# Optimization experiments

Measured on AMD Instinct MI355X. Metric: run time of the kernel, lower is better.

The kernel has to match this reference:

```python
import jax, jax.numpy as jnp
import numpy as np
from jax import lax

B, H, W, C = 2, 256, 256, 180
WS, SH, NH = 8, 4, 6
HD = C // NH          # 30
N = WS * WS           # 64
NW = (H // WS) * (W // WS)
HID = 4 * C
SCALE = HD ** -0.5
EPS = 1e-5


def _rel_pos_index(ws):
    coords = np.stack(np.meshgrid(np.arange(ws), np.arange(ws), indexing='ij'))  # [2,ws,ws]
    cf = coords.reshape(2, -1)
    rel = (cf[:, :, None] - cf[:, None, :]).transpose(1, 2, 0)  # [N,N,2]
    rel[:, :, 0] += ws - 1
    rel[:, :, 1] += ws - 1
    rel[:, :, 0] *= 2 * ws - 1
    return rel.sum(-1)  # [N,N]


def _attn_mask(h, w, ws, sh):
    img = np.zeros((h, w))
    sl = (slice(0, -ws), slice(-ws, -sh), slice(-sh, None))
    cnt = 0
    for hs in sl:
        for wsl in sl:
            img[hs, wsl] = cnt
            cnt += 1
    mw = img.reshape(h // ws, ws, w // ws, ws).transpose(0, 2, 1, 3).reshape(-1, ws * ws)  # [nW,N]
    d = mw[:, None, :] - mw[:, :, None]  # [nW,N,N]
    return np.where(d != 0, -100.0, 0.0).astype(np.float32)


REL_IDX = jnp.asarray(_rel_pos_index(WS))          # [N,N] int
MASK = jnp.asarray(_attn_mask(H, W, WS, SH))       # [nW,N,N] float


def _ln(x, g, b):
    m = jnp.mean(x, -1, keepdims=True)
    v = jnp.mean((x - m) ** 2, -1, keepdims=True)
    return (x - m) * lax.rsqrt(v + EPS) * g + b


def _win_part(x):  # (B,H,W,C) -> (B*nW,N,C)
    x = x.reshape(B, H // WS, WS, W // WS, WS, C).transpose(0, 1, 3, 2, 4, 5)
    return x.reshape(-1, N, C)


def _win_rev(w):  # (B*nW,N,C) -> (B,H,W,C)
    x = w.reshape(B, H // WS, W // WS, WS, WS, C).transpose(0, 1, 3, 2, 4, 5)
    return x.reshape(B, H, W, C)


def setup_inputs() -> dict:
    key = jax.random.key(0)
    ks = jax.random.split(key, 8)
    s = 0.02
    return {
        'x': jax.random.normal(ks[0], (B, H * W, C), jnp.float32),
        'norm1_g': jnp.ones((C,), jnp.float32),
        'norm1_b': jnp.zeros((C,), jnp.float32),
        'qkv_w': jax.random.normal(ks[1], (C, 3 * C), jnp.float32) * s,
        'qkv_b': jnp.zeros((3 * C,), jnp.float32),
        'rel_pos_table': jax.random.normal(ks[2], ((2 * WS - 1) ** 2, NH), jnp.float32) * s,
        'proj_w': jax.random.normal(ks[3], (C, C), jnp.float32) * s,
        'proj_b': jnp.zeros((C,), jnp.float32),
        'norm2_g': jnp.ones((C,), jnp.float32),
        'norm2_b': jnp.zeros((C,), jnp.float32),
        'fc1_w': jax.random.normal(ks[4], (C, HID), jnp.float32) * s,
        'fc1_b': jnp.zeros((HID,), jnp.float32),
        'dw_w': jax.random.normal(ks[5], (HID, 1, 3, 3), jnp.float32) * s,
        'dw_b': jnp.zeros((HID,), jnp.float32),
        'fc2_w': jax.random.normal(ks[6], (HID, C), jnp.float32) * s,
        'fc2_b': jnp.zeros((C,), jnp.float32),
    }


def reference(x, norm1_g, norm1_b, qkv_w, qkv_b, rel_pos_table, proj_w, proj_b,
              norm2_g, norm2_b, fc1_w, fc1_b, dw_w, dw_b, fc2_w, fc2_b):
    shortcut = x
    h = _ln(x, norm1_g, norm1_b).reshape(B, H, W, C)
    h = jnp.roll(h, (-SH, -SH), axis=(1, 2))           # cyclic shift
    xw = _win_part(h)                                   # [B*nW, N, C]

    qkv = (xw @ qkv_w + qkv_b).reshape(-1, N, 3, NH, HD).transpose(2, 0, 3, 1, 4)
    q, k, v = qkv[0] * SCALE, qkv[1], qkv[2]            # [B_,NH,N,HD]
    attn = jnp.einsum('bhnd,bhmd->bhnm', q, k)          # [B_,NH,N,N]

    bias = rel_pos_table[REL_IDX.reshape(-1)].reshape(N, N, NH).transpose(2, 0, 1)
    attn = attn + bias[None]
    attn = attn.reshape(B, NW, NH, N, N) + MASK[None, :, None]
    attn = jax.nn.softmax(attn.reshape(-1, NH, N, N), axis=-1)

    out = jnp.einsum('bhnm,bhmd->bhnd', attn, v).transpose(0, 2, 1, 3).reshape(-1, N, C)
    out = out @ proj_w + proj_b
    out = jnp.roll(_win_rev(out), (SH, SH), axis=(1, 2)).reshape(B, H * W, C)
    x = shortcut + out

    # MLP with depthwise-conv interleave
    m = _ln(x, norm2_g, norm2_b)
    m = jax.nn.gelu(m @ fc1_w + fc1_b, approximate=False)   # [B,L,HID]
    mc = m.transpose(0, 2, 1).reshape(B, HID, H, W)
    mc = lax.conv_general_dilated(mc, dw_w, (1, 1), 'SAME',
                                  feature_group_count=HID,
                                  dimension_numbers=('NCHW', 'OIHW', 'NCHW'))
    mc = mc + dw_b[None, :, None, None]
    m = jax.nn.gelu(mc.reshape(B, HID, H * W).transpose(0, 2, 1), approximate=False)
    m = m @ fc2_w + fc2_b
    return x + m
```

## Files before the change

kernel.cpp:

```cpp
#include <hip/hip_runtime.h>
#include <hip/hip_bf16.h>


using short8 = __attribute__((ext_vector_type(8))) short;
using f32x4  = __attribute__((ext_vector_type(4))) float;

constexpr int   ROWS   = 131072;
constexpr float SCALE_ = 0.18257418583505536f;

constexpr size_t OFF_WQ    = 0;
constexpr size_t OFF_WP    = OFF_WQ  + 576*192*2;
constexpr size_t OFF_WF1   = OFF_WP  + 192*192*2;
constexpr size_t OFF_WF2   = OFF_WF1 + 768*192*2;
constexpr size_t OFF_BQ    = OFF_WF2 + 192*736*2;
constexpr size_t OFF_BP    = OFF_BQ  + 576*4;
constexpr size_t OFF_BF1   = OFF_BP  + 192*4;
constexpr size_t OFF_BF2   = OFF_BF1 + 768*4;
constexpr size_t OFF_ZB    = OFF_BF2 + 192*4;
constexpr size_t OFF_BIASF = OFF_ZB  + 192*4;
constexpr size_t OFF_WDWT  = OFF_BIASF + 6*4096*4;
constexpr size_t OFF_BDW   = OFF_WDWT + 9*768*4;
constexpr size_t OFF_R1    = 1048576;
constexpr size_t SZ_R      = (size_t)ROWS * 192 * 2;
constexpr size_t OFF_R2    = OFF_R1 + SZ_R;
constexpr size_t OFF_R3    = OFF_R2 + SZ_R;
constexpr size_t WS_NEEDED = OFF_R3 + SZ_R;
static_assert(OFF_BDW + 768*4 <= OFF_R1, "weights overlap R1");

__device__ __forceinline__ unsigned short f2bf(float f) {
    __hip_bfloat16 h = __float2bfloat16(f);
    return *reinterpret_cast<unsigned short*>(&h);
}
__device__ __forceinline__ float bf2f(unsigned short u) {
    union { unsigned int i; float f; } x; x.i = ((unsigned int)u) << 16; return x.f;
}
__device__ __forceinline__ float gelu_f(float x) {
    return 0.5f * x * (1.0f + erff(x * 0.70710678118654752f));
}

__global__ __launch_bounds__(256) void prep_kernel(
    const float* __restrict__ qkv_w, const float* __restrict__ qkv_b,
    const float* __restrict__ proj_w, const float* __restrict__ proj_b,
    const float* __restrict__ fc1_w, const float* __restrict__ fc1_b,
    const float* __restrict__ fc2_w, const float* __restrict__ fc2_b,
    const float* __restrict__ rpt,
    const float* __restrict__ dw_w, const float* __restrict__ dw_b,
    unsigned short* __restrict__ wq, unsigned short* __restrict__ wp,
    unsigned short* __restrict__ wf1, unsigned short* __restrict__ wf2,
    float* __restrict__ bq, float* __restrict__ bp,
    float* __restrict__ bf1, float* __restrict__ bf2,
    float* __restrict__ zb, float* __restrict__ biasf,
    float* __restrict__ wdwT, float* __restrict__ bdw)
{
    int idx = blockIdx.x * 256 + threadIdx.x;
    constexpr int E1 = 576*192;
    constexpr int E2 = E1 + 192*192;
    constexpr int E3 = E2 + 768*192;
    constexpr int E4 = E3 + 192*736;
    constexpr int E5 = E4 + 576;
    constexpr int E6 = E5 + 192;
    constexpr int E7 = E6 + 768;
    constexpr int E8 = E7 + 192;
    constexpr int E8z = E8 + 192;
    constexpr int E9 = E8z + 6*4096;
    constexpr int E10 = E9 + 9*768;
    constexpr int E11 = E10 + 768;
    if (idx < E1) {
        int n = idx / 192, kx = idx % 192;
        float v = 0.f;
        if (n < 540 && kx < 180) { v = qkv_w[kx*540 + n]; if (n < 180) v *= SCALE_; }
        wq[idx] = f2bf(v);
    } else if (idx < E2) {
        int j = idx - E1; int n = j / 192, kx = j % 192;
        wp[j] = f2bf((n < 180 && kx < 180) ? proj_w[kx*180 + n] : 0.f);
    } else if (idx < E3) {
        int j = idx - E2; int n = j / 192, kx = j % 192;
        wf1[j] = f2bf((n < 720 && kx < 180) ? fc1_w[kx*720 + n] : 0.f);
    } else if (idx < E4) {
        int j = idx - E3; int n = j / 736, kx = j % 736;
        wf2[j] = f2bf((n < 180 && kx < 720) ? fc2_w[kx*180 + n] : 0.f);
    } else if (idx < E5) {
        int n = idx - E4;
        float v = (n < 540) ? qkv_b[n] : 0.f; if (n < 180) v *= SCALE_;
        bq[n] = v;
    } else if (idx < E6) {
        int n = idx - E5; bp[n] = (n < 180) ? proj_b[n] : 0.f;
    } else if (idx < E7) {
        int n = idx - E6; bf1[n] = (n < 720) ? fc1_b[n] : 0.f;
    } else if (idx < E8) {
        int n = idx - E7; bf2[n] = (n < 180) ? fc2_b[n] : 0.f;
    } else if (idx < E8z) {
        zb[idx - E8] = 0.f;
    } else if (idx < E9) {
        int j = idx - E8z;
        int hh = j / 4096, t = j & 4095;
        int n = t >> 6, m = t & 63;
        int rid = ((n>>3) - (m>>3) + 7)*15 + ((n&7) - (m&7) + 7);
        biasf[j] = rpt[rid*6 + hh];
    } else if (idx < E10) {
        int j = idx - E9;
        int tap = j / 768, c = j % 768;
        wdwT[j] = (c < 720) ? dw_w[c*9 + tap] : 0.f;
    } else if (idx < E11) {
        int c = idx - E10;
        bdw[c] = (c < 720) ? dw_b[c] : 0.f;
    }
}

template<int ROLL>
__global__ __launch_bounds__(256) void ln_kernel(const float* __restrict__ x,
    const float* __restrict__ g, const float* __restrict__ bsh,
    unsigned short* __restrict__ out)
{
    int row  = blockIdx.x * 4 + (threadIdx.x >> 6);
    int lane = threadIdx.x & 63;
    size_t src;
    if (ROLL) {
        int b    = row >> 16;
        int widx = (row >> 6) & 1023;
        int n    = row & 63;
        int hr   = ((widx >> 5) << 3) + (n >> 3);
        int wr   = ((widx & 31) << 3) + (n & 7);
        int h2   = (hr + 4) & 255;
        int w2   = (wr + 4) & 255;
        src = ((size_t)b << 16) + (h2 << 8) + w2;
    } else {
        src = (size_t)row;
    }
    const float* xr = x + src * 180;
    float v1 = xr[lane];
    float v2 = xr[lane + 64];
    float v3 = (lane < 52) ? xr[lane + 128] : 0.0f;
    float s1 = v1 + v2 + v3;
    float s2 = v1*v1 + v2*v2 + v3*v3;
    #pragma unroll
    for (int o = 32; o > 0; o >>= 1) { s1 += __shfl_xor(s1, o); s2 += __shfl_xor(s2, o); }
    float mean = s1 * (1.0f/180.0f);
    float var  = s2 * (1.0f/180.0f) - mean*mean;
    float rstd = rsqrtf(var + 1e-5f);
    unsigned short* orow = out + (size_t)row * 192;
    orow[lane]      = f2bf((v1 - mean)*rstd*g[lane]      + bsh[lane]);
    orow[lane + 64] = f2bf((v2 - mean)*rstd*g[lane + 64] + bsh[lane + 64]);
    if (lane < 52) orow[lane + 128] = f2bf((v3 - mean)*rstd*g[lane + 128] + bsh[lane + 128]);
    else           orow[lane + 128] = 0;
}

__global__ __launch_bounds__(256) void zeropad_kernel(unsigned int* q, unsigned int* k, unsigned int* v)
{
    int idx = blockIdx.x * 256 + threadIdx.x;
    int wid = idx / 192, t = idx % 192;
    if (t < 64)       q[wid*1024 + t*16 + 15] = 0;
    else if (t < 128) k[wid*1024 + (t-64)*16 + 15] = 0;
    else              v[wid*1024 + 960 + (t-128)] = 0;
}

template<int MODE>
__global__ __launch_bounds__(256) void gemm64(
    const unsigned short* __restrict__ A, const unsigned short* __restrict__ Bt,
    const float* __restrict__ bias, int K, int lda, int ldb,
    float* __restrict__ out_f, const float* __restrict__ xres,
    unsigned short* __restrict__ oq, unsigned short* __restrict__ ok2,
    unsigned short* __restrict__ ov, unsigned short* __restrict__ obf)
{
    __shared__ __align__(16) unsigned short As[64*40];
    __shared__ __align__(16) unsigned short Bs[64*40];
    const int tid  = threadIdx.x;
    const int bm   = blockIdx.x, bn = blockIdx.y;
    const int lane = tid & 63;
    const int wv   = tid >> 6;
    const int wr   = wv >> 1, wc = wv & 1;
    const int l15  = lane & 15, l4 = lane >> 4;
    const int r    = tid >> 2;
    const int kk   = (tid & 3) << 3;

    f32x4 acc[2][2];
    #pragma unroll
    for (int i = 0; i < 2; i++)
        #pragma unroll
        for (int j = 0; j < 2; j++) acc[i][j] = f32x4{0.f, 0.f, 0.f, 0.f};

    const size_t abase = (size_t)(bm*64 + r) * (size_t)lda + kk;
    const size_t bbase = (size_t)(bn*64 + r) * (size_t)ldb + kk;
    const int lds_wi = r*40 + kk;

    for (int kt = 0; kt < K; kt += 32) {
        *(uint4*)&As[lds_wi] = *(const uint4*)&A[abase + kt];
        *(uint4*)&Bs[lds_wi] = *(const uint4*)&Bt[bbase + kt];
        __syncthreads();
        short8 af[2], bf[2];
        #pragma unroll
        for (int fm = 0; fm < 2; fm++) af[fm] = *(const short8*)&As[(wr*32 + fm*16 + l15)*40 + l4*8];
        #pragma unroll
        for (int fn = 0; fn < 2; fn++) bf[fn] = *(const short8*)&Bs[(wc*32 + fn*16 + l15)*40 + l4*8];
        #pragma unroll
        for (int fm = 0; fm < 2; fm++)
            #pragma unroll
            for (int fn = 0; fn < 2; fn++)
                acc[fm][fn] = __builtin_amdgcn_mfma_f32_16x16x32_bf16(af[fm], bf[fn], acc[fm][fn], 0, 0, 0);
        __syncthreads();
    }

    #pragma unroll
    for (int fm = 0; fm < 2; fm++) {
      #pragma unroll
      for (int fn = 0; fn < 2; fn++) {
        #pragma unroll
        for (int rr = 0; rr < 4; rr++) {
            int row_l = wr*32 + fm*16 + l4*4 + rr;
            int col_l = wc*32 + fn*16 + l15;
            int grow  = bm*64 + row_l;
            int gcol  = bn*64 + col_l;
            float v = acc[fm][fn][rr] + bias[gcol];
            if (MODE == 0) {
                if (gcol < 540) {
                    int which = (gcol >= 360) ? 2 : (gcol >= 180 ? 1 : 0);
                    int cc = gcol - which*180;
                    int hh = cc / 30;
                    int dd = cc - hh*30;
                    size_t wid = (size_t)(grow >> 6)*6 + hh;
                    if (which == 0)      oq [wid*2048 + (grow & 63)*32 + dd] = f2bf(v);
                    else if (which == 1) ok2[wid*2048 + (grow & 63)*32 + dd] = f2bf(v);
                    else                 ov [wid*2048 + dd*64 + (grow & 63)] = f2bf(v);
                }
            } else if (MODE == 1) {
                if (gcol < 180) {
                    int b    = grow >> 16;
                    int widx = (grow >> 6) & 1023;
                    int n    = grow & 63;
                    int hr   = ((widx >> 5) << 3) + (n >> 3);
                    int wr2  = ((widx & 31) << 3) + (n & 7);
                    int h2   = (hr + 4) & 255;
                    int w2   = (wr2 + 4) & 255;
                    size_t orow = ((size_t)b << 16) + (h2 << 8) + w2;
                    out_f[orow*180 + gcol] = xres[orow*180 + gcol] + v;
                }
            } else if (MODE == 2) {
                obf[(size_t)grow*192 + gcol] = f2bf(gelu_f(v));
            } else {
                if (gcol < 180) out_f[(size_t)grow*180 + gcol] += v;
            }
        }
      }
    }
}

__global__ __launch_bounds__(64) void attn_kernel(
    const unsigned short* __restrict__ q, const unsigned short* __restrict__ k,
    const unsigned short* __restrict__ vt, const float* __restrict__ biasf,
    unsigned short* __restrict__ aout)
{
    __shared__ __align__(16) unsigned short P[64*72];
    const int wid  = blockIdx.x;
    const int b_   = wid / 6, hh = wid % 6;
    const int lane = threadIdx.x;
    const int l15  = lane & 15, l4 = lane >> 4;

    const unsigned short* qb = q  + (size_t)wid*2048;
    const unsigned short* kb = k  + (size_t)wid*2048;
    const unsigned short* vb = vt + (size_t)wid*2048;

    short8 qf[4], kf[4];
    #pragma unroll
    for (int t = 0; t < 4; t++) {
        qf[t] = *(const short8*)&qb[(t*16 + l15)*32 + l4*8];
        kf[t] = *(const short8*)&kb[(t*16 + l15)*32 + l4*8];
    }
    f32x4 s[4][4];
    #pragma unroll
    for (int m = 0; m < 4; m++)
        #pragma unroll
        for (int n = 0; n < 4; n++)
            s[m][n] = __builtin_amdgcn_mfma_f32_16x16x32_bf16(qf[m], kf[n], f32x4{0.f,0.f,0.f,0.f}, 0, 0, 0);

    const int wi = b_ & 1023;
    const int wh = wi >> 5, ww = wi & 31;
    const bool edge = (wh == 31) || (ww == 31);
    const float* bh = biasf + hh*4096;
    #pragma unroll
    for (int m = 0; m < 4; m++) {
      #pragma unroll
      for (int rr = 0; rr < 4; rr++) {
        int ni = m*16 + l4*4 + rr;
        int ln_n = 0;
        if (edge) {
            int rh = (wh < 31) ? 0 : (((ni >> 3) < 4) ? 1 : 2);
            int rw = (ww < 31) ? 0 : (((ni & 7) < 4) ? 1 : 2);
            ln_n = rh*3 + rw;
        }
        #pragma unroll
        for (int n = 0; n < 4; n++) {
            int mj = n*16 + l15;
            float add = bh[ni*64 + mj];
            if (edge) {
                int rh = (wh < 31) ? 0 : (((mj >> 3) < 4) ? 1 : 2);
                int rw = (ww < 31) ? 0 : (((mj & 7) < 4) ? 1 : 2);
                if (rh*3 + rw != ln_n) add -= 100.0f;
            }
            s[m][n][rr] += add;
        }
      }
    }
    #pragma unroll
    for (int m = 0; m < 4; m++) {
      #pragma unroll
      for (int rr = 0; rr < 4; rr++) {
        float mx = fmaxf(fmaxf(s[m][0][rr], s[m][1][rr]), fmaxf(s[m][2][rr], s[m][3][rr]));
        #pragma unroll
        for (int o = 8; o > 0; o >>= 1) mx = fmaxf(mx, __shfl_xor(mx, o));
        float sum = 0.f;
        #pragma unroll
        for (int n = 0; n < 4; n++) { float e = __expf(s[m][n][rr] - mx); s[m][n][rr] = e; sum += e; }
        #pragma unroll
        for (int o = 8; o > 0; o >>= 1) sum += __shfl_xor(sum, o);
        float inv = 1.0f / sum;
        int ni = m*16 + l4*4 + rr;
        #pragma unroll
        for (int n = 0; n < 4; n++) P[ni*72 + n*16 + l15] = f2bf(s[m][n][rr] * inv);
      }
    }
    __syncthreads();
    f32x4 po[4][2];
    #pragma unroll
    for (int m = 0; m < 4; m++)
        #pragma unroll
        for (int n = 0; n < 2; n++) po[m][n] = f32x4{0.f,0.f,0.f,0.f};
    #pragma unroll
    for (int ks = 0; ks < 2; ks++) {
        short8 pf[4], vf[2];
        #pragma unroll
        for (int m = 0; m < 4; m++) pf[m] = *(const short8*)&P[(m*16 + l15)*72 + ks*32 + l4*8];
        #pragma unroll
        for (int n = 0; n < 2; n++) vf[n] = *(const short8*)&vb[(n*16 + l15)*64 + ks*32 + l4*8];
        #pragma unroll
        for (int m = 0; m < 4; m++)
            #pragma unroll
            for (int n = 0; n < 2; n++)
                po[m][n] = __builtin_amdgcn_mfma_f32_16x16x32_bf16(pf[m], vf[n], po[m][n], 0, 0, 0);
    }
    #pragma unroll
    for (int m = 0; m < 4; m++)
      #pragma unroll
      for (int n = 0; n < 2; n++)
        #pragma unroll
        for (int rr = 0; rr < 4; rr++) {
            int ni = m*16 + l4*4 + rr;
            int dd = n*16 + l15;
            if (dd < 30)
                aout[((size_t)b_*64 + ni)*192 + hh*30 + dd] = f2bf(po[m][n][rr]);
        }
}

__global__ __launch_bounds__(192) void dwconv_kernel(
    const unsigned short* __restrict__ m1, const float* __restrict__ wT,
    const float* __restrict__ bias, int c0, unsigned short* __restrict__ m2)
{
    const int rowid = blockIdx.x;
    const int b   = rowid >> 8;
    const int hh  = rowid & 255;
    const int t   = threadIdx.x;
    const int cg  = t % 24;
    const int pl  = t / 24;
    const int w0  = blockIdx.y * 64 + pl * 8;
    const int c   = cg * 8;
    const int cgl = c0 + c;

    float acc[8][8];
    float bv[8];
    *(f32x4*)&bv[0] = *(const f32x4*)&bias[cgl];
    *(f32x4*)&bv[4] = *(const f32x4*)&bias[cgl + 4];
    #pragma unroll
    for (int p = 0; p < 8; p++)
        #pragma unroll
        for (int i = 0; i < 8; i++) acc[p][i] = bv[i];

    const short8 zv = {0,0,0,0,0,0,0,0};
    #pragma unroll
    for (int dh = -1; dh <= 1; dh++) {
        int h2 = hh + dh;
        if (h2 < 0 || h2 > 255) continue;
        const unsigned short* rb = m1 + ((size_t)(b*65536 + h2*256))*192 + c;
        float f[10][8];
        #pragma unroll
        for (int j = 0; j < 10; j++) {
            int w2 = w0 - 1 + j;
            short8 v = (w2 < 0 || w2 > 255) ? zv : *(const short8*)&rb[(size_t)w2*192];
            #pragma unroll
            for (int i = 0; i < 8; i++) f[j][i] = bf2f((unsigned short)v[i]);
        }
        #pragma unroll
        for (int dw2 = 0; dw2 < 3; dw2++) {
            const float* wrow = wT + ((dh+1)*3 + dw2)*768 + cgl;
            float wt[8];
            *(f32x4*)&wt[0] = *(const f32x4*)&wrow[0];
            *(f32x4*)&wt[4] = *(const f32x4*)&wrow[4];
            #pragma unroll
            for (int p = 0; p < 8; p++)
                #pragma unroll
                for (int i = 0; i < 8; i++)
                    acc[p][i] += f[p + dw2][i] * wt[i];
        }
    }
    unsigned short* ob = m2 + ((size_t)(b*65536 + hh*256))*192 + c;
    #pragma unroll
    for (int p = 0; p < 8; p++) {
        short8 o;
        #pragma unroll
        for (int i = 0; i < 8; i++) o[i] = (short)f2bf(gelu_f(acc[p][i]));
        *(short8*)&ob[(size_t)(w0 + p)*192] = o;
    }
}

extern "C" void kernel_launch(void* const* d_in, const int* in_sizes, int n_in,
                              void* d_out, int out_size, void* d_ws, size_t ws_size,
                              hipStream_t stream) {
    (void)in_sizes; (void)n_in; (void)out_size;
    if (ws_size < WS_NEEDED) return;
    const float* x      = (const float*)d_in[0];
    const float* n1g    = (const float*)d_in[1];
    const float* n1b    = (const float*)d_in[2];
    const float* qkv_w  = (const float*)d_in[3];
    const float* qkv_b  = (const float*)d_in[4];
    const float* rpt    = (const float*)d_in[5];
    const float* proj_w = (const float*)d_in[6];
    const float* proj_b = (const float*)d_in[7];
    const float* n2g    = (const float*)d_in[8];
    const float* n2b    = (const float*)d_in[9];
    const float* fc1_w  = (const float*)d_in[10];
    const float* fc1_b  = (const float*)d_in[11];
    const float* dw_w   = (const float*)d_in[12];
    const float* dw_b   = (const float*)d_in[13];
    const float* fc2_w  = (const float*)d_in[14];
    const float* fc2_b  = (const float*)d_in[15];
    float* out = (float*)d_out;
    char*  ws  = (char*)d_ws;

    unsigned short* wq   = (unsigned short*)(ws + OFF_WQ);
    unsigned short* wp   = (unsigned short*)(ws + OFF_WP);
    unsigned short* wf1  = (unsigned short*)(ws + OFF_WF1);
    unsigned short* wf2  = (unsigned short*)(ws + OFF_WF2);
    float* bq    = (float*)(ws + OFF_BQ);
    float* bp    = (float*)(ws + OFF_BP);
    float* bf1   = (float*)(ws + OFF_BF1);
    float* bf2   = (float*)(ws + OFF_BF2);
    float* zb    = (float*)(ws + OFF_ZB);
    float* biasf = (float*)(ws + OFF_BIASF);
    float* wdwT  = (float*)(ws + OFF_WDWT);
    float* bdw   = (float*)(ws + OFF_BDW);
    unsigned short* R1 = (unsigned short*)(ws + OFF_R1);
    unsigned short* R2 = (unsigned short*)(ws + OFF_R2);
    unsigned short* R3 = (unsigned short*)(ws + OFF_R3);
    unsigned short* qp = (unsigned short*)d_out;

    prep_kernel<<<1838, 256, 0, stream>>>(qkv_w, qkv_b, proj_w, proj_b, fc1_w, fc1_b,
                                          fc2_w, fc2_b, rpt, dw_w, dw_b,
                                          wq, wp, wf1, wf2,
                                          bq, bp, bf1, bf2, zb, biasf, wdwT, bdw);
    ln_kernel<1><<<32768, 256, 0, stream>>>(x, n1g, n1b, R1);
    gemm64<0><<<dim3(2048, 9), 256, 0, stream>>>(R1, wq, bq, 192, 192, 192,
                                                 nullptr, nullptr, qp, R2, R3, nullptr);
    zeropad_kernel<<<9216, 256, 0, stream>>>((unsigned int*)qp, (unsigned int*)R2, (unsigned int*)R3);
    attn_kernel<<<12288, 64, 0, stream>>>(qp, R2, R3, biasf, R1);
    gemm64<1><<<dim3(2048, 3), 256, 0, stream>>>(R1, wp, bp, 192, 192, 192,
                                                 out, x, nullptr, nullptr, nullptr, nullptr);
    ln_kernel<0><<<32768, 256, 0, stream>>>(out, n2g, n2b, R1);
    for (int q4 = 0; q4 < 4; ++q4) {
        gemm64<2><<<dim3(2048, 3), 256, 0, stream>>>(R1, wf1 + q4*192*192, bf1 + q4*192,
                                                     192, 192, 192,
                                                     nullptr, nullptr, nullptr, nullptr, nullptr, R2);
        dwconv_kernel<<<dim3(512, 4), 192, 0, stream>>>(R2, wdwT, bdw, q4*192, R3);
        gemm64<3><<<dim3(2048, 3), 256, 0, stream>>>(R3, wf2 + q4*192, (q4 == 0) ? bf2 : zb,
                                                     192, 192, 736,
                                                     out, nullptr, nullptr, nullptr, nullptr, nullptr);
    }
}
```

Measured before the change: 1.013 ms.

## Restructure MLP into spatial bands over full hidden width

The MLP used to be processed in four 192-channel chunks over the whole image. It now runs over eight 64-row spatial bands, each covering the full 768-wide hidden dimension with a one-row halo for the depthwise conv. Each band runs fc1, then the conv, then a single fc2 GEMM with K=768. This removes the repeated read-modify-write of the fp32 output across four fc2 passes and keeps each band's intermediates small enough to stay cache-resident. The cost is recomputing halo rows in fc1, more kernel launches, and smaller grids for fc2 (256x3 blocks per band).

```diff
diff --git a/kernel.cpp b/kernel.cpp
--- a/kernel.cpp
+++ b/kernel.cpp
@@ -9,15 +9,14 @@
 constexpr float SCALE_ = 0.18257418583505536f;
 
 constexpr size_t OFF_WQ    = 0;
-constexpr size_t OFF_WP    = OFF_WQ  + 576*192*2;
-constexpr size_t OFF_WF1   = OFF_WP  + 192*192*2;
-constexpr size_t OFF_WF2   = OFF_WF1 + 768*192*2;
-constexpr size_t OFF_BQ    = OFF_WF2 + 192*736*2;
-constexpr size_t OFF_BP    = OFF_BQ  + 576*4;
-constexpr size_t OFF_BF1   = OFF_BP  + 192*4;
-constexpr size_t OFF_BF2   = OFF_BF1 + 768*4;
-constexpr size_t OFF_ZB    = OFF_BF2 + 192*4;
-constexpr size_t OFF_BIASF = OFF_ZB  + 192*4;
+constexpr size_t OFF_WP    = OFF_WQ   + 576*192*2;
+constexpr size_t OFF_WF1   = OFF_WP   + 192*192*2;
+constexpr size_t OFF_WF2T  = OFF_WF1  + 768*192*2;
+constexpr size_t OFF_BQ    = OFF_WF2T + 192*768*2;
+constexpr size_t OFF_BP    = OFF_BQ   + 576*4;
+constexpr size_t OFF_BF1   = OFF_BP   + 192*4;
+constexpr size_t OFF_BF2   = OFF_BF1  + 768*4;
+constexpr size_t OFF_BIASF = OFF_BF2  + 192*4;
 constexpr size_t OFF_WDWT  = OFF_BIASF + 6*4096*4;
 constexpr size_t OFF_BDW   = OFF_WDWT + 9*768*4;
 constexpr size_t OFF_R1    = 1048576;
@@ -26,6 +25,7 @@
 constexpr size_t OFF_R3    = OFF_R2 + SZ_R;
 constexpr size_t WS_NEEDED = OFF_R3 + SZ_R;
 static_assert(OFF_BDW + 768*4 <= OFF_R1, "weights overlap R1");
+static_assert((size_t)66*256*768*2 <= SZ_R, "m1 band overflows R2");
 
 __device__ __forceinline__ unsigned short f2bf(float f) {
     __hip_bfloat16 h = __float2bfloat16(f);
@@ -46,23 +46,22 @@
     const float* __restrict__ rpt,
     const float* __restrict__ dw_w, const float* __restrict__ dw_b,
     unsigned short* __restrict__ wq, unsigned short* __restrict__ wp,
-    unsigned short* __restrict__ wf1, unsigned short* __restrict__ wf2,
+    unsigned short* __restrict__ wf1, unsigned short* __restrict__ wf2t,
     float* __restrict__ bq, float* __restrict__ bp,
     float* __restrict__ bf1, float* __restrict__ bf2,
-    float* __restrict__ zb, float* __restrict__ biasf,
+    float* __restrict__ biasf,
     float* __restrict__ wdwT, float* __restrict__ bdw)
 {
     int idx = blockIdx.x * 256 + threadIdx.x;
     constexpr int E1 = 576*192;
     constexpr int E2 = E1 + 192*192;
     constexpr int E3 = E2 + 768*192;
-    constexpr int E4 = E3 + 192*736;
+    constexpr int E4 = E3 + 192*768;
     constexpr int E5 = E4 + 576;
     constexpr int E6 = E5 + 192;
     constexpr int E7 = E6 + 768;
     constexpr int E8 = E7 + 192;
-    constexpr int E8z = E8 + 192;
-    constexpr int E9 = E8z + 6*4096;
+    constexpr int E9 = E8 + 6*4096;
     constexpr int E10 = E9 + 9*768;
     constexpr int E11 = E10 + 768;
     if (idx < E1) {
@@ -77,8 +76,8 @@
         int j = idx - E2; int n = j / 192, kx = j % 192;
         wf1[j] = f2bf((n < 720 && kx < 180) ? fc1_w[kx*720 + n] : 0.f);
     } else if (idx < E4) {
-        int j = idx - E3; int n = j / 736, kx = j % 736;
-        wf2[j] = f2bf((n < 180 && kx < 720) ? fc2_w[kx*180 + n] : 0.f);
+        int j = idx - E3; int n = j / 768, kx = j % 768;
+        wf2t[j] = f2bf((n < 180 && kx < 720) ? fc2_w[kx*180 + n] : 0.f);
     } else if (idx < E5) {
         int n = idx - E4;
         float v = (n < 540) ? qkv_b[n] : 0.f; if (n < 180) v *= SCALE_;
@@ -89,10 +88,8 @@
         int n = idx - E6; bf1[n] = (n < 720) ? fc1_b[n] : 0.f;
     } else if (idx < E8) {
         int n = idx - E7; bf2[n] = (n < 180) ? fc2_b[n] : 0.f;
-    } else if (idx < E8z) {
-        zb[idx - E8] = 0.f;
     } else if (idx < E9) {
-        int j = idx - E8z;
+        int j = idx - E8;
         int hh = j / 4096, t = j & 4095;
         int n = t >> 6, m = t & 63;
         int rid = ((n>>3) - (m>>3) + 7)*15 + ((n&7) - (m&7) + 7);
@@ -157,7 +154,7 @@
 template<int MODE>
 __global__ __launch_bounds__(256) void gemm64(
     const unsigned short* __restrict__ A, const unsigned short* __restrict__ Bt,
-    const float* __restrict__ bias, int K, int lda, int ldb,
+    const float* __restrict__ bias, int K, int lda, int ldb, int ldo,
     float* __restrict__ out_f, const float* __restrict__ xres,
     unsigned short* __restrict__ oq, unsigned short* __restrict__ ok2,
     unsigned short* __restrict__ ov, unsigned short* __restrict__ obf)
@@ -235,7 +232,7 @@
                     out_f[orow*180 + gcol] = xres[orow*180 + gcol] + v;
                 }
             } else if (MODE == 2) {
-                obf[(size_t)grow*192 + gcol] = f2bf(gelu_f(v));
+                obf[(size_t)grow*ldo + gcol] = f2bf(gelu_f(v));
             } else {
                 if (gcol < 180) out_f[(size_t)grow*180 + gcol] += v;
             }
@@ -350,24 +347,21 @@
         }
 }
 
-__global__ __launch_bounds__(192) void dwconv_kernel(
+__global__ __launch_bounds__(256) void dwconv_band(
     const unsigned short* __restrict__ m1, const float* __restrict__ wT,
-    const float* __restrict__ bias, int c0, unsigned short* __restrict__ m2)
-{
-    const int rowid = blockIdx.x;
-    const int b   = rowid >> 8;
-    const int hh  = rowid & 255;
+    const float* __restrict__ bias, int h0, unsigned short* __restrict__ m2)
+{
+    const int hl  = blockIdx.x;
     const int t   = threadIdx.x;
-    const int cg  = t % 24;
-    const int pl  = t / 24;
+    const int cg  = t & 31;
+    const int pl  = t >> 5;
     const int w0  = blockIdx.y * 64 + pl * 8;
-    const int c   = cg * 8;
-    const int cgl = c0 + c;
+    const int c   = blockIdx.z * 256 + cg * 8;
 
     float acc[8][8];
     float bv[8];
-    *(f32x4*)&bv[0] = *(const f32x4*)&bias[cgl];
-    *(f32x4*)&bv[4] = *(const f32x4*)&bias[cgl + 4];
+    *(f32x4*)&bv[0] = *(const f32x4*)&bias[c];
+    *(f32x4*)&bv[4] = *(const f32x4*)&bias[c + 4];
     #pragma unroll
     for (int p = 0; p < 8; p++)
         #pragma unroll
@@ -376,20 +370,20 @@
     const short8 zv = {0,0,0,0,0,0,0,0};
     #pragma unroll
     for (int dh = -1; dh <= 1; dh++) {
-        int h2 = hh + dh;
-        if (h2 < 0 || h2 > 255) continue;
-        const unsigned short* rb = m1 + ((size_t)(b*65536 + h2*256))*192 + c;
+        int hg = h0 + hl + dh;
+        if (hg < 0 || hg > 255) continue;
+        const unsigned short* rb = m1 + (size_t)(hl + 1 + dh) * 256 * 768 + c;
         float f[10][8];
         #pragma unroll
         for (int j = 0; j < 10; j++) {
             int w2 = w0 - 1 + j;
-            short8 v = (w2 < 0 || w2 > 255) ? zv : *(const short8*)&rb[(size_t)w2*192];
+            short8 v = (w2 < 0 || w2 > 255) ? zv : *(const short8*)&rb[(size_t)w2*768];
             #pragma unroll
             for (int i = 0; i < 8; i++) f[j][i] = bf2f((unsigned short)v[i]);
         }
         #pragma unroll
         for (int dw2 = 0; dw2 < 3; dw2++) {
-            const float* wrow = wT + ((dh+1)*3 + dw2)*768 + cgl;
+            const float* wrow = wT + ((dh+1)*3 + dw2)*768 + c;
             float wt[8];
             *(f32x4*)&wt[0] = *(const f32x4*)&wrow[0];
             *(f32x4*)&wt[4] = *(const f32x4*)&wrow[4];
@@ -400,13 +394,13 @@
                     acc[p][i] += f[p + dw2][i] * wt[i];
         }
     }
-    unsigned short* ob = m2 + ((size_t)(b*65536 + hh*256))*192 + c;
+    unsigned short* ob = m2 + ((size_t)hl*256 + w0)*768 + c;
     #pragma unroll
     for (int p = 0; p < 8; p++) {
         short8 o;
         #pragma unroll
         for (int i = 0; i < 8; i++) o[i] = (short)f2bf(gelu_f(acc[p][i]));
-        *(short8*)&ob[(size_t)(w0 + p)*192] = o;
+        *(short8*)&ob[(size_t)p*768] = o;
     }
 }
 
@@ -437,12 +431,11 @@
     unsigned short* wq   = (unsigned short*)(ws + OFF_WQ);
     unsigned short* wp   = (unsigned short*)(ws + OFF_WP);
     unsigned short* wf1  = (unsigned short*)(ws + OFF_WF1);
-    unsigned short* wf2  = (unsigned short*)(ws + OFF_WF2);
+    unsigned short* wf2t = (unsigned short*)(ws + OFF_WF2T);
     float* bq    = (float*)(ws + OFF_BQ);
     float* bp    = (float*)(ws + OFF_BP);
     float* bf1   = (float*)(ws + OFF_BF1);
     float* bf2   = (float*)(ws + OFF_BF2);
-    float* zb    = (float*)(ws + OFF_ZB);
     float* biasf = (float*)(ws + OFF_BIASF);
     float* wdwT  = (float*)(ws + OFF_WDWT);
     float* bdw   = (float*)(ws + OFF_BDW);
@@ -451,25 +444,33 @@
     unsigned short* R3 = (unsigned short*)(ws + OFF_R3);
     unsigned short* qp = (unsigned short*)d_out;
 
-    prep_kernel<<<1838, 256, 0, stream>>>(qkv_w, qkv_b, proj_w, proj_b, fc1_w, fc1_b,
+    prep_kernel<<<1861, 256, 0, stream>>>(qkv_w, qkv_b, proj_w, proj_b, fc1_w, fc1_b,
                                           fc2_w, fc2_b, rpt, dw_w, dw_b,
-                                          wq, wp, wf1, wf2,
-                                          bq, bp, bf1, bf2, zb, biasf, wdwT, bdw);
+                                          wq, wp, wf1, wf2t,
+                                          bq, bp, bf1, bf2, biasf, wdwT, bdw);
     ln_kernel<1><<<32768, 256, 0, stream>>>(x, n1g, n1b, R1);
-    gemm64<0><<<dim3(2048, 9), 256, 0, stream>>>(R1, wq, bq, 192, 192, 192,
+    gemm64<0><<<dim3(2048, 9), 256, 0, stream>>>(R1, wq, bq, 192, 192, 192, 0,
                                                  nullptr, nullptr, qp, R2, R3, nullptr);
     zeropad_kernel<<<9216, 256, 0, stream>>>((unsigned int*)qp, (unsigned int*)R2, (unsigned int*)R3);
     attn_kernel<<<12288, 64, 0, stream>>>(qp, R2, R3, biasf, R1);
-    gemm64<1><<<dim3(2048, 3), 256, 0, stream>>>(R1, wp, bp, 192, 192, 192,
+    gemm64<1><<<dim3(2048, 3), 256, 0, stream>>>(R1, wp, bp, 192, 192, 192, 0,
                                                  out, x, nullptr, nullptr, nullptr, nullptr);
     ln_kernel<0><<<32768, 256, 0, stream>>>(out, n2g, n2b, R1);
-    for (int q4 = 0; q4 < 4; ++q4) {
-        gemm64<2><<<dim3(2048, 3), 256, 0, stream>>>(R1, wf1 + q4*192*192, bf1 + q4*192,
-                                                     192, 192, 192,
-                                                     nullptr, nullptr, nullptr, nullptr, nullptr, R2);
-        dwconv_kernel<<<dim3(512, 4), 192, 0, stream>>>(R2, wdwT, bdw, q4*192, R3);
-        gemm64<3><<<dim3(2048, 3), 256, 0, stream>>>(R3, wf2 + q4*192, (q4 == 0) ? bf2 : zb,
-                                                     192, 192, 736,
-                                                     out, nullptr, nullptr, nullptr, nullptr, nullptr);
-    }
-}
+    for (int band = 0; band < 8; ++band) {
+        const int b_img   = band >> 2;
+        const int h0      = (band & 3) * 64;
+        const int h_start = (h0 == 0) ? 0 : h0 - 1;
+        const int h_end   = (h0 + 64 < 256) ? (h0 + 65) : 256;
+        const int n_rows  = h_end - h_start;
+        const int moff    = (h0 == 0) ? 1 : 0;
+        const size_t arow0 = ((size_t)b_img*256 + h_start) * 256;
+        const size_t pix0  = ((size_t)b_img*256 + h0) * 256;
+        gemm64<2><<<dim3(n_rows*4, 12), 256, 0, stream>>>(
+            R1 + arow0*192, wf1, bf1, 192, 192, 192, 768,
+            nullptr, nullptr, nullptr, nullptr, nullptr, R2 + (size_t)moff*256*768);
+        dwconv_band<<<dim3(64, 4, 3), 256, 0, stream>>>(R2, wdwT, bdw, h0, R3);
+        gemm64<3><<<dim3(256, 3), 256, 0, stream>>>(
+            R3, wf2t, bf2, 768, 768, 768, 0,
+            out + pix0*180, nullptr, nullptr, nullptr, nullptr, nullptr);
+    }
+}
```

Result: faster. 897.7 us (-11.4%).
